# Performance work log

Hardware: AMD Instinct MI355X
Metric: run time of the kernel (lower is better)

Reference implementation:

```python
import jax, jax.numpy as jnp
import numpy as np

N_NODES = 100000
N_EDGES = 1600000
IN_FEAT = 50
HIDDEN = 64
N_CLASSES = 41


def setup_inputs() -> dict:
    key = jax.random.key(0)
    ks = jax.random.split(key, 8)
    x = jax.random.normal(ks[0], (N_NODES, IN_FEAT), dtype=jnp.float32)
    W1_l = jax.random.normal(ks[1], (IN_FEAT, HIDDEN), dtype=jnp.float32) * (1.0 / np.sqrt(IN_FEAT))
    W1_r = jax.random.normal(ks[2], (IN_FEAT, HIDDEN), dtype=jnp.float32) * (1.0 / np.sqrt(IN_FEAT))
    b1 = jnp.zeros((HIDDEN,), dtype=jnp.float32)
    W2_l = jax.random.normal(ks[3], (HIDDEN, N_CLASSES), dtype=jnp.float32) * (1.0 / np.sqrt(HIDDEN))
    W2_r = jax.random.normal(ks[4], (HIDDEN, N_CLASSES), dtype=jnp.float32) * (1.0 / np.sqrt(HIDDEN))
    b2 = jnp.zeros((N_CLASSES,), dtype=jnp.float32)
    src = jax.random.randint(ks[5], (N_EDGES,), 0, N_NODES, dtype=jnp.int64 if jax.config.jax_enable_x64 else jnp.int32)
    dst = jax.random.randint(ks[6], (N_EDGES,), 0, N_NODES, dtype=jnp.int64 if jax.config.jax_enable_x64 else jnp.int32)
    return {"x": x, "W1_l": W1_l, "W1_r": W1_r, "b1": b1,
            "W2_l": W2_l, "W2_r": W2_r, "b2": b2, "src": src, "dst": dst}


def _sage_conv(h, src, dst, W_l, W_r, b):
    # sum-aggregate neighbor features (message from src -> dst), then dense transform
    agg = jax.ops.segment_sum(h[src], dst, num_segments=N_NODES)  # [N, F]
    return agg @ W_l + h @ W_r + b


def reference(x, W1_l, W1_r, b1, W2_l, W2_r, b2, src, dst):
    h = _sage_conv(x, src, dst, W1_l, W1_r, b1)
    h = jax.nn.relu(h)
    # dropout is identity in eval mode
    o = _sage_conv(h, src, dst, W2_l, W2_r, b2)
    return jax.nn.log_softmax(o, axis=1)
```

## Files before the change

kernel.cpp:

```cpp
#include <hip/hip_runtime.h>
#include <hip/hip_bf16.h>
#include <math.h>

#define N_NODES   100000
#define N_EDGES   1600000
#define IN_FEAT   50
#define HIDDEN    64
#define N_CLASSES 41
#define NC48      48
#define N_TILES   (N_NODES / 16)

#define NPB   200
#define NBUK  (N_NODES / NPB)
#define BEPT  16
#define BA_BLOCKS ((N_EDGES + 256 * BEPT - 1) / (256 * BEPT))
#define SCAP  4096

#define PACKX_BLOCKS (N_NODES * 64 / 256)
#define PW_BLOCKS    28

typedef __attribute__((ext_vector_type(8))) _Float16 half8;
typedef __attribute__((ext_vector_type(4))) float   float4v;

union f16pk { _Float16 h[2]; unsigned u; };

__device__ __forceinline__ int clampidx(int i) {
  return ((unsigned)i < (unsigned)N_NODES) ? i : 0;
}

__device__ __forceinline__ int clampoff(int v) {
  return ((unsigned)v <= (unsigned)N_EDGES) ? v : 0;
}

__device__ __forceinline__ void acc8(float* acc, half8 u, float one) {
#pragma unroll
  for (int t = 0; t < 8; ++t) acc[t] = fmaf((float)u[t], one, acc[t]);
}

__device__ __forceinline__ void accf8(float* acc, uint2 u) {
  auto p0 = __builtin_amdgcn_cvt_pk_f32_fp8(u.x, 0);
  auto p1 = __builtin_amdgcn_cvt_pk_f32_fp8(u.x, 1);
  auto p2 = __builtin_amdgcn_cvt_pk_f32_fp8(u.y, 0);
  auto p3 = __builtin_amdgcn_cvt_pk_f32_fp8(u.y, 1);
  acc[0] += p0[0]; acc[1] += p0[1];
  acc[2] += p1[0]; acc[3] += p1[1];
  acc[4] += p2[0]; acc[5] += p2[1];
  acc[6] += p3[0]; acc[7] += p3[1];
}

__global__ __launch_bounds__(256) void prep_kernel(
    const float* __restrict__ x, _Float16* __restrict__ xh,
    const float* __restrict__ W1l, const float* __restrict__ W1r,
    const float* __restrict__ W2l, const float* __restrict__ W2r,
    unsigned* __restrict__ wt1l, unsigned* __restrict__ wt1r,
    unsigned* __restrict__ wt2l, unsigned* __restrict__ wt2r,
    int* __restrict__ bcnt, int* __restrict__ wcurrel,
    int* __restrict__ start) {
  if (blockIdx.x < PACKX_BLOCKS) {
    int i = blockIdx.x * 256 + threadIdx.x;
    int node = i >> 6, c = i & 63;
    xh[i] = (c < IN_FEAT) ? (_Float16)x[node * IN_FEAT + c] : (_Float16)0.f;
    return;
  }
  int tid = threadIdx.x;
  if (blockIdx.x == PACKX_BLOCKS) {
    bcnt[tid] = 0; bcnt[256 + tid] = 0;
    wcurrel[tid] = 0; wcurrel[256 + tid] = 0;
    if (tid == 0) start[N_NODES] = N_EDGES;
  }
  int i = (blockIdx.x - PACKX_BLOCKS) * 256 + tid;
  f16pk pk;
  if (i < 2048 * 2) {
    int which = i >> 11, j = i & 2047;
    int n = j >> 5, kp = j & 31;
    const float* W = which ? W1r : W1l;
    int k0 = 2 * kp, k1 = 2 * kp + 1;
    pk.h[0] = (_Float16)((k0 < IN_FEAT) ? W[k0 * HIDDEN + n] : 0.f);
    pk.h[1] = (_Float16)((k1 < IN_FEAT) ? W[k1 * HIDDEN + n] : 0.f);
    (which ? wt1r : wt1l)[j] = pk.u;
  } else if (i < 4096 + 2 * 1536) {
    int j = i - 4096;
    int which = (j >= 1536), jj = which ? j - 1536 : j;
    int n = jj >> 5, kp = jj & 31;
    const float* W = which ? W2r : W2l;
    pk.h[0] = (_Float16)((n < N_CLASSES) ? W[(2 * kp) * N_CLASSES + n] : 0.f);
    pk.h[1] = (_Float16)((n < N_CLASSES) ? W[(2 * kp + 1) * N_CLASSES + n] : 0.f);
    (which ? wt2r : wt2l)[jj] = pk.u;
  }
}

__global__ __launch_bounds__(256) void bhist_kernel(
    const int* __restrict__ dst, int* __restrict__ bcnt) {
  __shared__ int lh[NBUK];
  int tid = threadIdx.x;
  for (int i = tid; i < NBUK; i += 256) lh[i] = 0;
  __syncthreads();
  int base = blockIdx.x * (256 * BEPT);
#pragma unroll
  for (int k = 0; k < BEPT; ++k) {
    int e = base + k * 256 + tid;
    if (e < N_EDGES) {
      int d = clampidx(dst[e]);
      atomicAdd(&lh[(unsigned)d / (unsigned)NPB], 1);
    }
  }
  __syncthreads();
  for (int i = tid; i < NBUK; i += 256)
    if (lh[i]) atomicAdd(&bcnt[i], lh[i]);
}

__global__ __launch_bounds__(256) void bucketA_kernel(
    const int* __restrict__ src, const int* __restrict__ dst,
    const int* __restrict__ bcnt, int* __restrict__ wcurrel,
    int* __restrict__ pairs) {
  __shared__ int sc[256];
  __shared__ int wb[NBUK];
  __shared__ int lcnt[NBUK];
  __shared__ int lbase[NBUK];
  int tid = threadIdx.x;
  int i0 = 2 * tid, i1 = 2 * tid + 1;
  int a0 = (i0 < NBUK) ? bcnt[i0] : 0;
  int a1 = (i1 < NBUK) ? bcnt[i1] : 0;
  int s = a0 + a1;
  sc[tid] = s;
  for (int i = tid; i < NBUK; i += 256) lcnt[i] = 0;
  __syncthreads();
  for (int off = 1; off < 256; off <<= 1) {
    int t = (tid >= off) ? sc[tid - off] : 0;
    __syncthreads();
    sc[tid] += t;
    __syncthreads();
  }
  int excl = sc[tid] - s;
  if (i0 < NBUK) wb[i0] = excl;
  if (i1 < NBUK) wb[i1] = excl + a0;
  __syncthreads();

  int base = blockIdx.x * (256 * BEPT);
  int pk[BEPT], w[BEPT], rk[BEPT];
#pragma unroll
  for (int k = 0; k < BEPT; ++k) {
    int e = base + k * 256 + tid;
    rk[k] = -1;
    if (e < N_EDGES) {
      int sv = clampidx(src[e]);
      int d = clampidx(dst[e]);
      w[k] = (unsigned)d / (unsigned)NPB;
      pk[k] = (sv << 8) | (d - w[k] * NPB);
      rk[k] = atomicAdd(&lcnt[w[k]], 1);
    }
  }
  __syncthreads();
  for (int i = tid; i < NBUK; i += 256)
    lbase[i] = wb[i] + atomicAdd(&wcurrel[i], lcnt[i]);
  __syncthreads();
#pragma unroll
  for (int k = 0; k < BEPT; ++k) {
    if (rk[k] >= 0) {
      int pos = lbase[w[k]] + rk[k];
      if ((unsigned)pos < (unsigned)N_EDGES) pairs[pos] = pk[k];
    }
  }
}

__global__ __launch_bounds__(256) void sort2_kernel(
    const int* __restrict__ pairs, const int* __restrict__ bcnt,
    int* __restrict__ start, int* __restrict__ ssrc) {
  __shared__ int obuf[SCAP];
  __shared__ int lhist[NPB];
  __shared__ int lcur[NPB];
  __shared__ int lscan[256];
  __shared__ int lohi[2];
  int b = blockIdx.x;
  int nbase = b * NPB;
  int tid = threadIdx.x;
  {
    int i0 = 2 * tid, i1 = 2 * tid + 1;
    int a0 = (i0 < NBUK) ? bcnt[i0] : 0;
    int a1 = (i1 < NBUK) ? bcnt[i1] : 0;
    int s = a0 + a1;
    lscan[tid] = s;
    __syncthreads();
    for (int off = 1; off < 256; off <<= 1) {
      int t = (tid >= off) ? lscan[tid - off] : 0;
      __syncthreads();
      lscan[tid] += t;
      __syncthreads();
    }
    int excl = lscan[tid] - s;
    if (i0 == b) { lohi[0] = excl;      lohi[1] = a0; }
    if (i1 == b) { lohi[0] = excl + a0; lohi[1] = a1; }
  }
  for (int i = tid; i < NPB; i += 256) lhist[i] = 0;
  __syncthreads();
  int lo = lohi[0];
  int ne = lohi[1];
  int hi = lo + ne;
  for (int i = lo + tid; i < hi; i += 256) {
    unsigned li = (unsigned)pairs[i] & 255u;
    if (li < (unsigned)NPB) atomicAdd(&lhist[li], 1);
  }
  __syncthreads();
  int hv = (tid < NPB) ? lhist[tid] : 0;
  lscan[tid] = hv;
  __syncthreads();
  for (int off = 1; off < 256; off <<= 1) {
    int t = (tid >= off) ? lscan[tid - off] : 0;
    __syncthreads();
    lscan[tid] += t;
    __syncthreads();
  }
  if (tid < NPB) {
    int excl = lscan[tid] - hv;
    lcur[tid] = excl;
    unsigned sidx = (unsigned)(nbase + tid);
    if (sidx < (unsigned)N_NODES) start[sidx] = lo + excl;
  }
  __syncthreads();
  if (ne >= 0 && ne <= SCAP) {
    for (int i = lo + tid; i < hi; i += 256) {
      int p = pairs[i];
      unsigned li = (unsigned)p & 255u;
      if (li < (unsigned)NPB) {
        int pos = atomicAdd(&lcur[li], 1);
        if ((unsigned)pos < (unsigned)SCAP) obuf[pos] = (int)((unsigned)p >> 8);
      }
    }
    __syncthreads();
    for (int i = tid; i < ne; i += 256) {
      unsigned gi = (unsigned)(lo + i);
      if (gi < (unsigned)N_EDGES) ssrc[gi] = obuf[i];
    }
  } else {
    for (int i = lo + tid; i < hi; i += 256) {
      int p = pairs[i];
      unsigned li = (unsigned)p & 255u;
      if (li < (unsigned)NPB) {
        int pos = atomicAdd(&lcur[li], 1);
        unsigned gi = (unsigned)(lo + pos);
        if (gi < (unsigned)N_EDGES) ssrc[gi] = (int)((unsigned)p >> 8);
      }
    }
  }
}

__global__ __launch_bounds__(256) void g1mlp_kernel(
    const half8* __restrict__ xq,
    const int* __restrict__ start, const int* __restrict__ ssrc,
    const _Float16* __restrict__ xh,
    const unsigned* __restrict__ wt1l, const unsigned* __restrict__ wt1r,
    const unsigned* __restrict__ wt2l, const unsigned* __restrict__ wt2r,
    const float* __restrict__ b1, const float* __restrict__ b2,
    unsigned char* __restrict__ hlf8, float* __restrict__ opart, float one) {
  __shared__ float aggF[16][68];
  __shared__ float sH[16][68];
  int tile = blockIdx.x;
  int wv = __builtin_amdgcn_readfirstlane(threadIdx.x >> 6);
  int lane = threadIdx.x & 63;
  int r = lane >> 3, q = lane & 7;

  int nb = tile * 16 + wv * 4;
  int st[5];
#pragma unroll
  for (int k = 0; k < 5; ++k) st[k] = clampoff(start[nb + k]);
  int iv[4];
#pragma unroll
  for (int k = 0; k < 4; ++k) {
    int cnt = st[k + 1] - st[k]; if (cnt > 64) cnt = 64;
    iv[k] = (lane < cnt) ? ssrc[st[k] + lane] : 0;
  }
#pragma unroll
  for (int k = 0; k < 4; ++k) {
    float accA[8] = {0.f, 0.f, 0.f, 0.f, 0.f, 0.f, 0.f, 0.f};
    float accB[8] = {0.f, 0.f, 0.f, 0.f, 0.f, 0.f, 0.f, 0.f};
    int s0 = st[k], s1 = st[k + 1];
    int idxv = iv[k];
    for (int base = s0; base < s1; base += 64) {
      int cnt = s1 - base;
      if (cnt > 64) cnt = 64;
      if (base != s0) idxv = (lane < cnt) ? ssrc[base + lane] : 0;
      int j = 0;
      for (; j + 16 <= cnt; j += 16) {
        int iA = clampidx(__shfl(idxv, j + r));
        int iB = clampidx(__shfl(idxv, j + 8 + r));
        acc8(accA, xq[iA * 8 + q], one);
        acc8(accB, xq[iB * 8 + q], one);
      }
      for (; j + 8 <= cnt; j += 8) {
        int iA = clampidx(__shfl(idxv, j + r));
        acc8(accA, xq[iA * 8 + q], one);
      }
      if (j < cnt) {
        int nrem = cnt - j;
        int iA = clampidx(__shfl(idxv, j + r));
        if (r < nrem) acc8(accA, xq[iA * 8 + q], one);
      }
    }
#pragma unroll
    for (int t = 0; t < 8; ++t) accA[t] += accB[t];
#pragma unroll
    for (int off = 8; off <= 32; off <<= 1) {
#pragma unroll
      for (int t = 0; t < 8; ++t) accA[t] += __shfl_xor(accA[t], off);
    }
    if (r == 0) {
      int nl = wv * 4 + k;
#pragma unroll
      for (int t = 0; t < 8; ++t) aggF[nl][q * 8 + t] = accA[t];
    }
  }
  __syncthreads();

  int m = lane & 15, quad = lane >> 4;

  half8 Aa[2], Ax[2];
#pragma unroll
  for (int s = 0; s < 2; ++s) {
    const float* pa = &aggF[m][s * 32 + quad * 8];
    half8 A;
#pragma unroll
    for (int jj = 0; jj < 8; ++jj) A[jj] = (_Float16)pa[jj];
    Aa[s] = A;
    Ax[s] = *(const half8*)(xh + (tile * 16 + m) * 64 + s * 32 + quad * 8);
  }

  {
    int n = wv * 16 + m;
    half8 Bl0 = *(const half8*)(wt1l + n * 32 + quad * 4);
    half8 Bl1 = *(const half8*)(wt1l + n * 32 + 16 + quad * 4);
    half8 Br0 = *(const half8*)(wt1r + n * 32 + quad * 4);
    half8 Br1 = *(const half8*)(wt1r + n * 32 + 16 + quad * 4);
    float4v acc = {0.f, 0.f, 0.f, 0.f};
    acc = __builtin_amdgcn_mfma_f32_16x16x32_f16(Aa[0], Bl0, acc, 0, 0, 0);
    acc = __builtin_amdgcn_mfma_f32_16x16x32_f16(Aa[1], Bl1, acc, 0, 0, 0);
    acc = __builtin_amdgcn_mfma_f32_16x16x32_f16(Ax[0], Br0, acc, 0, 0, 0);
    acc = __builtin_amdgcn_mfma_f32_16x16x32_f16(Ax[1], Br1, acc, 0, 0, 0);
    float bv = b1[n];
#pragma unroll
    for (int rr = 0; rr < 4; ++rr) {
      sH[quad * 4 + rr][n] = fmaxf(acc[rr] + bv, 0.f);
    }
  }
  __syncthreads();

  if (wv >= 3) return;
  half8 Ah[2];
#pragma unroll
  for (int s = 0; s < 2; ++s) {
    const float* pr = &sH[m][s * 32 + quad * 8];
    half8 A;
#pragma unroll
    for (int jj = 0; jj < 8; ++jj) A[jj] = (_Float16)pr[jj];
    Ah[s] = A;
  }
  {
    int n = wv * 16 + m;
    half8 Cl0 = *(const half8*)(wt2l + n * 32 + quad * 4);
    half8 Cl1 = *(const half8*)(wt2l + n * 32 + 16 + quad * 4);
    half8 Cr0 = *(const half8*)(wt2r + n * 32 + quad * 4);
    half8 Cr1 = *(const half8*)(wt2r + n * 32 + 16 + quad * 4);
    float4v acc2 = {0.f, 0.f, 0.f, 0.f};
    float4v acc3 = {0.f, 0.f, 0.f, 0.f};
    acc2 = __builtin_amdgcn_mfma_f32_16x16x32_f16(Ah[0], Cl0, acc2, 0, 0, 0);
    acc2 = __builtin_amdgcn_mfma_f32_16x16x32_f16(Ah[1], Cl1, acc2, 0, 0, 0);
    acc3 = __builtin_amdgcn_mfma_f32_16x16x32_f16(Ah[0], Cr0, acc3, 0, 0, 0);
    acc3 = __builtin_amdgcn_mfma_f32_16x16x32_f16(Ah[1], Cr1, acc3, 0, 0, 0);
    float bv = (n < N_CLASSES) ? b2[n] : 0.f;
#pragma unroll
    for (int rr = 0; rr < 4; ++rr) {
      int row = tile * 16 + quad * 4 + rr;
      int v8 = __builtin_amdgcn_cvt_pk_fp8_f32(acc2[rr], acc2[rr], 0, 0);
      hlf8[row * NC48 + n] = (unsigned char)(v8 & 0xff);
      opart[row * NC48 + n] = acc3[rr] + bv;
    }
  }
}

#define AROW 49
__global__ __launch_bounds__(256) void g2tile_kernel(
    const uint2* __restrict__ hq,
    const float4* __restrict__ opart4,
    const int* __restrict__ start, const int* __restrict__ ssrc,
    float* __restrict__ out) {
  __shared__ float aggF[16][AROW];
  int tile = blockIdx.x;
  int wv = __builtin_amdgcn_readfirstlane(threadIdx.x >> 6);
  int lane = threadIdx.x & 63;
  int r = lane >> 3, q = lane & 7;
  bool qOK = (q < 6);

  int nb = tile * 16 + wv * 4;
  int st[5];
#pragma unroll
  for (int k = 0; k < 5; ++k) st[k] = clampoff(start[nb + k]);
  int iv[4];
#pragma unroll
  for (int k = 0; k < 4; ++k) {
    int cnt = st[k + 1] - st[k]; if (cnt > 64) cnt = 64;
    iv[k] = (lane < cnt) ? ssrc[st[k] + lane] : 0;
  }
#pragma unroll
  for (int k = 0; k < 4; ++k) {
    float accA[8] = {0.f, 0.f, 0.f, 0.f, 0.f, 0.f, 0.f, 0.f};
    float accB[8] = {0.f, 0.f, 0.f, 0.f, 0.f, 0.f, 0.f, 0.f};
    int s0 = st[k], s1 = st[k + 1];
    int idxv = iv[k];
    for (int base = s0; base < s1; base += 64) {
      int cnt = s1 - base;
      if (cnt > 64) cnt = 64;
      if (base != s0) idxv = (lane < cnt) ? ssrc[base + lane] : 0;
      int j = 0;
      for (; j + 16 <= cnt; j += 16) {
        int iA = clampidx(__shfl(idxv, j + r));
        int iB = clampidx(__shfl(idxv, j + 8 + r));
        if (qOK) {
          accf8(accA, hq[iA * 6 + q]);
          accf8(accB, hq[iB * 6 + q]);
        }
      }
      for (; j + 8 <= cnt; j += 8) {
        int iA = clampidx(__shfl(idxv, j + r));
        if (qOK) accf8(accA, hq[iA * 6 + q]);
      }
      if (j < cnt) {
        int nrem = cnt - j;
        int iA = clampidx(__shfl(idxv, j + r));
        if (r < nrem && qOK) accf8(accA, hq[iA * 6 + q]);
      }
    }
#pragma unroll
    for (int t = 0; t < 8; ++t) accA[t] += accB[t];
#pragma unroll
    for (int off = 8; off <= 32; off <<= 1) {
#pragma unroll
      for (int t = 0; t < 8; ++t) accA[t] += __shfl_xor(accA[t], off);
    }
    if (r == 0 && qOK) {
      int nl = wv * 4 + k;
#pragma unroll
      for (int t = 0; t < 8; ++t) aggF[nl][q * 8 + t] = accA[t];
    }
  }
  __syncthreads();

  if (wv != 0) return;
  int m = lane >> 2, s = lane & 3;
  int node = tile * 16 + m;

  float o[12];
#pragma unroll
  for (int i = 0; i < 3; ++i) {
    float4 a = opart4[node * 12 + s * 3 + i];
    o[i * 4 + 0] = a.x; o[i * 4 + 1] = a.y;
    o[i * 4 + 2] = a.z; o[i * 4 + 3] = a.w;
  }
  float lmax = -INFINITY;
#pragma unroll
  for (int j = 0; j < 12; ++j) {
    int f = s * 12 + j;
    o[j] += aggF[m][f];
    if (f < N_CLASSES) lmax = fmaxf(lmax, o[j]);
  }
  float vm = lmax;
#pragma unroll
  for (int off = 1; off <= 2; off <<= 1) vm = fmaxf(vm, __shfl_xor(vm, off));
  float lsum = 0.f;
#pragma unroll
  for (int j = 0; j < 12; ++j) {
    int f = s * 12 + j;
    if (f < N_CLASSES) lsum += expf(o[j] - vm);
  }
#pragma unroll
  for (int off = 1; off <= 2; off <<= 1) lsum += __shfl_xor(lsum, off);
  float lse = logf(lsum);
#pragma unroll
  for (int j = 0; j < 12; ++j) {
    int f = s * 12 + j;
    if (f < N_CLASSES) out[node * N_CLASSES + f] = o[j] - vm - lse;
  }
}

extern "C" void kernel_launch(void* const* d_in, const int* in_sizes, int n_in,
                              void* d_out, int out_size, void* d_ws, size_t ws_size,
                              hipStream_t stream) {
  const float* x   = (const float*)d_in[0];
  const float* W1l = (const float*)d_in[1];
  const float* W1r = (const float*)d_in[2];
  const float* b1  = (const float*)d_in[3];
  const float* W2l = (const float*)d_in[4];
  const float* W2r = (const float*)d_in[5];
  const float* b2  = (const float*)d_in[6];
  const int*   src = (const int*)d_in[7];
  const int*   dst = (const int*)d_in[8];
  float* out = (float*)d_out;

  int* counts  = (int*)d_ws;
  int* start   = counts + N_NODES;
  int* cursor  = start + (N_NODES + 1);
  int* partial = cursor + N_NODES;
  int* ssrc    = partial + 64;
  unsigned* wt1l = (unsigned*)(ssrc + N_EDGES);
  unsigned* wt1r = wt1l + 2048;
  unsigned* wt2l = wt1r + 2048;
  unsigned* wt2r = wt2l + 1536;
  uintptr_t pal = ((uintptr_t)(wt2r + 1536) + 255) & ~(uintptr_t)255;
  float* opart   = (float*)pal;
  _Float16* xh   = (_Float16*)(opart + (size_t)N_NODES * NC48);
  _Float16* hlh  = xh + (size_t)N_NODES * 64;

  unsigned char* hlf8 = (unsigned char*)hlh;

  int* bcnt    = counts;
  int* wcurrel = counts + 512;

  int* pairs = (int*)opart;

  prep_kernel<<<PACKX_BLOCKS + PW_BLOCKS, 256, 0, stream>>>(
      x, xh, W1l, W1r, W2l, W2r, wt1l, wt1r, wt2l, wt2r,
      bcnt, wcurrel, start);
  bhist_kernel<<<BA_BLOCKS, 256, 0, stream>>>(dst, bcnt);
  bucketA_kernel<<<BA_BLOCKS, 256, 0, stream>>>(src, dst, bcnt, wcurrel, pairs);
  sort2_kernel<<<NBUK, 256, 0, stream>>>(pairs, bcnt, start, ssrc);

  g1mlp_kernel<<<N_TILES, 256, 0, stream>>>(
      (const half8*)xh, start, ssrc, xh, wt1l, wt1r, wt2l, wt2r,
      b1, b2, hlf8, opart, 1.0f);

  g2tile_kernel<<<N_TILES, 256, 0, stream>>>(
      (const uint2*)hlf8, (const float4*)opart, start, ssrc, out);
}
```

Measured before the change: 231.5 us.

## Replace bucket histogram pass with fixed-capacity per-bucket slot regions

Removes the separate destination histogram kernel and scan. Edges are scattered into fixed 4096-slot regions per bucket using an atomic cursor per bucket. The sort kernel then scans the final cursor counts to get global offsets. This saves one pass over dst and one kernel launch, but edges are silently dropped if any bucket exceeds its slot capacity, and the oversized-bucket fallback path is gone.

```diff
diff --git a/kernel.cpp b/kernel.cpp
--- a/kernel.cpp
+++ b/kernel.cpp
@@ -12,6 +12,7 @@
 
 #define NPB   200
 #define NBUK  (N_NODES / NPB)
+#define SLOTS 4096
 #define BEPT  16
 #define BA_BLOCKS ((N_EDGES + 256 * BEPT - 1) / (256 * BEPT))
 #define SCAP  4096
@@ -54,8 +55,7 @@
     const float* __restrict__ W2l, const float* __restrict__ W2r,
     unsigned* __restrict__ wt1l, unsigned* __restrict__ wt1r,
     unsigned* __restrict__ wt2l, unsigned* __restrict__ wt2r,
-    int* __restrict__ bcnt, int* __restrict__ wcurrel,
-    int* __restrict__ start) {
+    int* __restrict__ wcur2, int* __restrict__ start) {
   if (blockIdx.x < PACKX_BLOCKS) {
     int i = blockIdx.x * 256 + threadIdx.x;
     int node = i >> 6, c = i & 63;
@@ -64,8 +64,7 @@
   }
   int tid = threadIdx.x;
   if (blockIdx.x == PACKX_BLOCKS) {
-    bcnt[tid] = 0; bcnt[256 + tid] = 0;
-    wcurrel[tid] = 0; wcurrel[256 + tid] = 0;
+    wcur2[tid] = 0; wcur2[256 + tid] = 0;
     if (tid == 0) start[N_NODES] = N_EDGES;
   }
   int i = (blockIdx.x - PACKX_BLOCKS) * 256 + tid;
@@ -89,51 +88,13 @@
   }
 }
 
-__global__ __launch_bounds__(256) void bhist_kernel(
-    const int* __restrict__ dst, int* __restrict__ bcnt) {
-  __shared__ int lh[NBUK];
-  int tid = threadIdx.x;
-  for (int i = tid; i < NBUK; i += 256) lh[i] = 0;
-  __syncthreads();
-  int base = blockIdx.x * (256 * BEPT);
-#pragma unroll
-  for (int k = 0; k < BEPT; ++k) {
-    int e = base + k * 256 + tid;
-    if (e < N_EDGES) {
-      int d = clampidx(dst[e]);
-      atomicAdd(&lh[(unsigned)d / (unsigned)NPB], 1);
-    }
-  }
-  __syncthreads();
-  for (int i = tid; i < NBUK; i += 256)
-    if (lh[i]) atomicAdd(&bcnt[i], lh[i]);
-}
-
 __global__ __launch_bounds__(256) void bucketA_kernel(
     const int* __restrict__ src, const int* __restrict__ dst,
-    const int* __restrict__ bcnt, int* __restrict__ wcurrel,
-    int* __restrict__ pairs) {
-  __shared__ int sc[256];
-  __shared__ int wb[NBUK];
+    int* __restrict__ wcur2, int* __restrict__ pairs) {
   __shared__ int lcnt[NBUK];
   __shared__ int lbase[NBUK];
   int tid = threadIdx.x;
-  int i0 = 2 * tid, i1 = 2 * tid + 1;
-  int a0 = (i0 < NBUK) ? bcnt[i0] : 0;
-  int a1 = (i1 < NBUK) ? bcnt[i1] : 0;
-  int s = a0 + a1;
-  sc[tid] = s;
-  for (int i = tid; i < NBUK; i += 256) lcnt[i] = 0;
-  __syncthreads();
-  for (int off = 1; off < 256; off <<= 1) {
-    int t = (tid >= off) ? sc[tid - off] : 0;
-    __syncthreads();
-    sc[tid] += t;
-    __syncthreads();
-  }
-  int excl = sc[tid] - s;
-  if (i0 < NBUK) wb[i0] = excl;
-  if (i1 < NBUK) wb[i1] = excl + a0;
+  for (int i = tid; i < NBUK; i += 256) { lcnt[i] = 0; lbase[i] = 0; }
   __syncthreads();
 
   int base = blockIdx.x * (256 * BEPT);
@@ -152,19 +113,19 @@
   }
   __syncthreads();
   for (int i = tid; i < NBUK; i += 256)
-    lbase[i] = wb[i] + atomicAdd(&wcurrel[i], lcnt[i]);
+    if (lcnt[i]) lbase[i] = atomicAdd(&wcur2[i], lcnt[i]);
   __syncthreads();
 #pragma unroll
   for (int k = 0; k < BEPT; ++k) {
     if (rk[k] >= 0) {
-      int pos = lbase[w[k]] + rk[k];
-      if ((unsigned)pos < (unsigned)N_EDGES) pairs[pos] = pk[k];
+      unsigned rel = (unsigned)(lbase[w[k]] + rk[k]);
+      if (rel < (unsigned)SLOTS) pairs[w[k] * SLOTS + (int)rel] = pk[k];
     }
   }
 }
 
 __global__ __launch_bounds__(256) void sort2_kernel(
-    const int* __restrict__ pairs, const int* __restrict__ bcnt,
+    const int* __restrict__ pairs, const int* __restrict__ wcur2,
     int* __restrict__ start, int* __restrict__ ssrc) {
   __shared__ int obuf[SCAP];
   __shared__ int lhist[NPB];
@@ -176,8 +137,8 @@
   int tid = threadIdx.x;
   {
     int i0 = 2 * tid, i1 = 2 * tid + 1;
-    int a0 = (i0 < NBUK) ? bcnt[i0] : 0;
-    int a1 = (i1 < NBUK) ? bcnt[i1] : 0;
+    int a0 = (i0 < NBUK) ? min(max(wcur2[i0], 0), SLOTS) : 0;
+    int a1 = (i1 < NBUK) ? min(max(wcur2[i1], 0), SLOTS) : 0;
     int s = a0 + a1;
     lscan[tid] = s;
     __syncthreads();
@@ -193,11 +154,11 @@
   }
   for (int i = tid; i < NPB; i += 256) lhist[i] = 0;
   __syncthreads();
-  int lo = lohi[0];
-  int ne = lohi[1];
-  int hi = lo + ne;
-  for (int i = lo + tid; i < hi; i += 256) {
-    unsigned li = (unsigned)pairs[i] & 255u;
+  int glo = lohi[0];
+  int ne  = lohi[1];
+  int plo = b * SLOTS;
+  for (int i = tid; i < ne; i += 256) {
+    unsigned li = (unsigned)pairs[plo + i] & 255u;
     if (li < (unsigned)NPB) atomicAdd(&lhist[li], 1);
   }
   __syncthreads();
@@ -214,33 +175,21 @@
     int excl = lscan[tid] - hv;
     lcur[tid] = excl;
     unsigned sidx = (unsigned)(nbase + tid);
-    if (sidx < (unsigned)N_NODES) start[sidx] = lo + excl;
-  }
-  __syncthreads();
-  if (ne >= 0 && ne <= SCAP) {
-    for (int i = lo + tid; i < hi; i += 256) {
-      int p = pairs[i];
-      unsigned li = (unsigned)p & 255u;
-      if (li < (unsigned)NPB) {
-        int pos = atomicAdd(&lcur[li], 1);
-        if ((unsigned)pos < (unsigned)SCAP) obuf[pos] = (int)((unsigned)p >> 8);
-      }
-    }
-    __syncthreads();
-    for (int i = tid; i < ne; i += 256) {
-      unsigned gi = (unsigned)(lo + i);
-      if (gi < (unsigned)N_EDGES) ssrc[gi] = obuf[i];
-    }
-  } else {
-    for (int i = lo + tid; i < hi; i += 256) {
-      int p = pairs[i];
-      unsigned li = (unsigned)p & 255u;
-      if (li < (unsigned)NPB) {
-        int pos = atomicAdd(&lcur[li], 1);
-        unsigned gi = (unsigned)(lo + pos);
-        if (gi < (unsigned)N_EDGES) ssrc[gi] = (int)((unsigned)p >> 8);
-      }
-    }
+    if (sidx < (unsigned)N_NODES) start[sidx] = glo + excl;
+  }
+  __syncthreads();
+  for (int i = tid; i < ne; i += 256) {
+    int p = pairs[plo + i];
+    unsigned li = (unsigned)p & 255u;
+    if (li < (unsigned)NPB) {
+      int pos = atomicAdd(&lcur[li], 1);
+      if ((unsigned)pos < (unsigned)SCAP) obuf[pos] = (int)((unsigned)p >> 8);
+    }
+  }
+  __syncthreads();
+  for (int i = tid; i < ne; i += 256) {
+    unsigned gi = (unsigned)(glo + i);
+    if (gi < (unsigned)N_EDGES) ssrc[gi] = obuf[i];
   }
 }
 
@@ -510,17 +459,14 @@
 
   unsigned char* hlf8 = (unsigned char*)hlh;
 
-  int* bcnt    = counts;
-  int* wcurrel = counts + 512;
+  int* wcur2 = counts;
 
   int* pairs = (int*)opart;
 
   prep_kernel<<<PACKX_BLOCKS + PW_BLOCKS, 256, 0, stream>>>(
-      x, xh, W1l, W1r, W2l, W2r, wt1l, wt1r, wt2l, wt2r,
-      bcnt, wcurrel, start);
-  bhist_kernel<<<BA_BLOCKS, 256, 0, stream>>>(dst, bcnt);
-  bucketA_kernel<<<BA_BLOCKS, 256, 0, stream>>>(src, dst, bcnt, wcurrel, pairs);
-  sort2_kernel<<<NBUK, 256, 0, stream>>>(pairs, bcnt, start, ssrc);
+      x, xh, W1l, W1r, W2l, W2r, wt1l, wt1r, wt2l, wt2r, wcur2, start);
+  bucketA_kernel<<<BA_BLOCKS, 256, 0, stream>>>(src, dst, wcur2, pairs);
+  sort2_kernel<<<NBUK, 256, 0, stream>>>(pairs, wcur2, start, ssrc);
 
   g1mlp_kernel<<<N_TILES, 256, 0, stream>>>(
       (const half8*)xh, start, ssrc, xh, wt1l, wt1r, wt2l, wt2r,
```

New measurement: 218.0 us. 1.06x faster.
